# Kernel optimization log

Measured on AMD Instinct MI355X. Metric: run time of the kernel, lower is better.

The kernel has to match this reference:

```python
import jax, jax.numpy as jnp
import numpy as np

H, D_MODEL, LEN_Q, LEN_K, D_K, D_V = 16, 1024, 2048, 2048, 64, 64
BATCH = 4
SCALE = 1.0 / np.sqrt(float(D_K))


def setup_inputs() -> dict:
    key = jax.random.key(0)
    ks = jax.random.split(key, 10)
    inp = {
        "Q": jax.random.normal(ks[0], (BATCH, LEN_Q, D_MODEL), dtype=jnp.float32),
        "K": jax.random.normal(ks[1], (BATCH, LEN_K, D_MODEL), dtype=jnp.float32),
        "V": jax.random.normal(ks[2], (BATCH, LEN_K, D_MODEL), dtype=jnp.float32),
        "mask": jax.random.randint(ks[3], (BATCH, LEN_K), 0, 2, dtype=jnp.int32),
        # Linear params (torch Linear: y = x @ W.T + b); store W as [in, out].
        "Wq": jax.random.normal(ks[4], (D_MODEL, H * D_K), dtype=jnp.float32) * (1.0 / np.sqrt(D_MODEL)),
        "bq": jnp.zeros((H * D_K,), dtype=jnp.float32),
        "Wk": jax.random.normal(ks[5], (D_MODEL, H * D_K), dtype=jnp.float32) * (1.0 / np.sqrt(D_MODEL)),
        "bk": jnp.zeros((H * D_K,), dtype=jnp.float32),
        "Wv": jax.random.normal(ks[6], (D_MODEL, H * D_V), dtype=jnp.float32) * (1.0 / np.sqrt(D_MODEL)),
        "bv": jnp.zeros((H * D_V,), dtype=jnp.float32),
    }
    return inp


def reference(Q, K, V, mask, Wq, bq, Wk, bk, Wv, bv):
    B = Q.shape[0]
    # Projections -> [B, S, H, d]
    q = (Q @ Wq + bq).reshape(B, LEN_Q, H, D_K)
    k = (K @ Wk + bk).reshape(B, LEN_K, H, D_K)
    v = (V @ Wv + bv).reshape(B, LEN_K, H, D_V)
    # Scores: [B, H, len_q, len_k]
    scores = jnp.einsum("bqhd,bkhd->bhqk", q, k) * SCALE
    # Key-padding mask broadcast over heads and queries
    scores = jnp.where(mask[:, None, None, :] == 0, jnp.float32(-1e9), scores)
    alpha = jax.nn.softmax(scores, axis=-1)
    out = jnp.einsum("bhqk,bkhd->bqhd", alpha, v)  # [B, len_q, H, d_v]
    return out.reshape(B, LEN_Q, H * D_V)
```

## Files before the change

### kernel.cpp

```cpp
#include <hip/hip_runtime.h>

#define NH 16
#define DM 1024
#define SQ 2048
#define BT 4

typedef __attribute__((ext_vector_type(8))) short bf16x8;
typedef __attribute__((ext_vector_type(4))) short sh4;
typedef __attribute__((ext_vector_type(4))) float f4;
typedef __attribute__((ext_vector_type(4))) float fv4;
typedef unsigned short u16;

#define M2BIAS 23.083120654f
#define SCALE2 0.18033688f

__device__ __forceinline__ u16 f2bf(float f) {
    union { float f; unsigned u; } v; v.f = f;
    unsigned r = v.u + 0x7FFFu + ((v.u >> 16) & 1u);
    return (u16)(r >> 16);
}

__device__ __forceinline__ float fast_exp2(float x) {
#if __has_builtin(__builtin_amdgcn_exp2f)
    return __builtin_amdgcn_exp2f(x);
#else
    return exp2f(x);
#endif
}

#if __has_builtin(__builtin_amdgcn_mfma_f32_16x16x16_bf16)
#define MFMA16(a, b, c) __builtin_amdgcn_mfma_f32_16x16x16_bf16(a, b, c, 0, 0, 0)
#elif __has_builtin(__builtin_amdgcn_mfma_f32_16x16x16bf16_1k)
#define MFMA16(a, b, c) __builtin_amdgcn_mfma_f32_16x16x16bf16_1k(a, b, c, 0, 0, 0)
#else
static __device__ __forceinline__ f4 mfma16_asm(sh4 a, sh4 b, f4 c) {
    asm("v_mfma_f32_16x16x16_bf16 %0, %1, %2, %0" : "+v"(c) : "v"(a), "v"(b));
    return c;
}
#define MFMA16(a, b, c) mfma16_asm(a, b, c)
#endif

#define GLD16(gp, lp) __builtin_amdgcn_global_load_lds( \
    (const __attribute__((address_space(1))) void*)(gp), \
    (__attribute__((address_space(3))) void*)(lp), 16, 0, 0)

__global__ __launch_bounds__(256) void cvt_x(const float* __restrict__ x, u16* __restrict__ y) {
    int i = blockIdx.x * 256 + threadIdx.x;
    fv4 v = ((const fv4*)x)[i];
    sh4 r;
    r[0] = (short)f2bf(v[0]); r[1] = (short)f2bf(v[1]);
    r[2] = (short)f2bf(v[2]); r[3] = (short)f2bf(v[3]);
    ((sh4*)y)[i] = r;
}

__global__ __launch_bounds__(256) void cvt_wT(const float* __restrict__ Wsrc, u16* __restrict__ Wt) {
    __shared__ float t[64][65];
    int r0 = blockIdx.x * 64, c0 = blockIdx.y * 64;
    #pragma unroll
    for (int i = 0; i < 16; ++i) {
        int idx = i * 256 + threadIdx.x;
        int r = idx >> 6, c = idx & 63;
        t[r][c] = Wsrc[(size_t)(r0 + r) * DM + c0 + c];
    }
    __syncthreads();
    #pragma unroll
    for (int i = 0; i < 16; ++i) {
        int idx = i * 256 + threadIdx.x;
        int n = idx >> 6, k = idx & 63;
        Wt[(size_t)(c0 + n) * DM + r0 + k] = f2bf(t[k][n]);
    }
}

__global__ __launch_bounds__(256) void mk_mbias(const int* __restrict__ mask, float* __restrict__ mb) {
    int i = blockIdx.x * 256 + threadIdx.x;
    mb[i] = mask[i] ? -M2BIAS : -__builtin_inff();
}

__global__ __launch_bounds__(256) void gemm_proj(const u16* __restrict__ A, const u16* __restrict__ Bt,
                                                 const float* __restrict__ bias, u16* __restrict__ outp,
                                                 int vmode) {
    __shared__ u16 As[128 * 64];
    __shared__ u16 Bs[128 * 64];
    int tid = threadIdx.x;
    int w = tid >> 6, lane = tid & 63, quad = lane >> 4, l16 = lane & 15;
    int wm = w >> 1, wn = w & 1;
    int r8 = lane >> 3, cg = (lane & 7) ^ r8;
    const u16* Ag = A + (size_t)blockIdx.x * 128 * DM;
    const u16* Bg = Bt + (size_t)blockIdx.y * 128 * DM;

    f4 acc[4][4];
    #pragma unroll
    for (int mt = 0; mt < 4; ++mt)
        #pragma unroll
        for (int nt = 0; nt < 4; ++nt) acc[mt][nt] = f4{0.f, 0.f, 0.f, 0.f};

    for (int kt = 0; kt < 16; ++kt) {
        int kofs = kt * 64 + cg * 8;
        #pragma unroll
        for (int c = 0; c < 4; ++c) {
            int rbase = w * 32 + c * 8;
            GLD16(Ag + (size_t)(rbase + r8) * DM + kofs, &As[rbase * 64]);
            GLD16(Bg + (size_t)(rbase + r8) * DM + kofs, &Bs[rbase * 64]);
        }
        __syncthreads();
        #pragma unroll
        for (int ks = 0; ks < 2; ++ks) {
            bf16x8 afr[4], bfr[4];
            #pragma unroll
            for (int mt = 0; mt < 4; ++mt) {
                int row = wm * 64 + mt * 16 + l16;
                int ch = (ks * 4 + quad) ^ (row & 7);
                afr[mt] = *(const bf16x8*)&As[row * 64 + ch * 8];
            }
            #pragma unroll
            for (int nt = 0; nt < 4; ++nt) {
                int row = wn * 64 + nt * 16 + l16;
                int ch = (ks * 4 + quad) ^ (row & 7);
                bfr[nt] = *(const bf16x8*)&Bs[row * 64 + ch * 8];
            }
            #pragma unroll
            for (int mt = 0; mt < 4; ++mt)
                #pragma unroll
                for (int nt = 0; nt < 4; ++nt)
                    acc[mt][nt] = __builtin_amdgcn_mfma_f32_16x16x32_bf16(afr[mt], bfr[nt], acc[mt][nt], 0, 0, 0);
        }
        __syncthreads();
    }

    #pragma unroll
    for (int nt = 0; nt < 4; ++nt) {
        int ncol = blockIdx.y * 128 + wn * 64 + nt * 16 + l16;
        float bn = bias[ncol];
        int h = ncol >> 6, d = ncol & 63;
        #pragma unroll
        for (int mt = 0; mt < 4; ++mt) {
            int mbase = blockIdx.x * 128 + wm * 64 + mt * 16 + quad * 4;
            int bidx = mbase >> 11, s0 = mbase & 2047;
            if (vmode == 0) {
                size_t base = ((size_t)bidx * NH + h) * SQ;
                #pragma unroll
                for (int reg = 0; reg < 4; ++reg)
                    outp[(base + s0 + reg) * 64 + d] = f2bf(acc[mt][nt][reg] + bn);
            } else {
                sh4 pk;
                #pragma unroll
                for (int reg = 0; reg < 4; ++reg) pk[reg] = (short)f2bf(acc[mt][nt][reg] + bn);
                *(sh4*)&outp[(((size_t)bidx * NH + h) * 64 + d) * SQ + s0] = pk;
            }
        }
    }
}

__global__ __launch_bounds__(256, 4) void attn(const u16* __restrict__ qw, const u16* __restrict__ kw,
                                               const u16* __restrict__ vtw, const float* __restrict__ mbias,
                                               float* __restrict__ outp) {
    __shared__ u16 Ks[2][64 * 64];
    __shared__ u16 Vs[2][64 * 64];
    int tid = threadIdx.x;
    int w = tid >> 6, lane = tid & 63, quad = lane >> 4, l16 = lane & 15;
    int r8 = lane >> 3, sl = lane & 7;
    int bh = blockIdx.x, b = bh >> 4;
    int h = bh & 15;
    int qbase = blockIdx.y * 128 + w * 32;
    const u16* qp = qw + (size_t)bh * SQ * 64;
    const u16* kp = kw + (size_t)bh * SQ * 64;
    const u16* vp = vtw + (size_t)bh * 64 * SQ;
    const float* mbp = mbias + b * SQ;

    bf16x8 aq[2][2];
    #pragma unroll
    for (int mt = 0; mt < 2; ++mt)
        #pragma unroll
        for (int ks = 0; ks < 2; ++ks)
            aq[mt][ks] = *(const bf16x8*)&qp[(size_t)(qbase + mt * 16 + l16) * 64 + ks * 32 + quad * 8];

    f4 o[2][4];
    float lrow[2] = {0.f, 0.f};
    #pragma unroll
    for (int mt = 0; mt < 2; ++mt)
        #pragma unroll
        for (int nt = 0; nt < 4; ++nt) o[mt][nt] = f4{0.f, 0.f, 0.f, 0.f};

    auto stage = [&](int buf, int k0) {
        #pragma unroll
        for (int j = 0; j < 2; ++j) {
            int row = w * 16 + j * 8 + r8;
            int gsl = sl ^ (row & 7);
            GLD16(kp + (size_t)(k0 + row) * 64 + gsl * 8, &Ks[buf][(w * 16 + j * 8) * 64]);
            GLD16(vp + (size_t)row * SQ + k0 + gsl * 8, &Vs[buf][(w * 16 + j * 8) * 64]);
        }
    };

    stage(0, 0);
    for (int kb = 0; kb < 32; ++kb) {
        int buf = kb & 1;
        int k0 = kb * 64;
        __syncthreads();
        fv4 bias4[4];
        #pragma unroll
        for (int kt = 0; kt < 4; ++kt)
            bias4[kt] = *(const fv4*)&mbp[k0 + kt * 16 + quad * 4];
        if (kb + 1 < 32) stage(buf ^ 1, k0 + 64);

        bf16x8 bk[4][2];
        #pragma unroll
        for (int kt = 0; kt < 4; ++kt)
            #pragma unroll
            for (int ks = 0; ks < 2; ++ks) {
                int r = kt * 16 + l16;
                int slot = (ks * 4 + quad) ^ (r & 7);
                bk[kt][ks] = *(const bf16x8*)&Ks[buf][r * 64 + slot * 8];
            }
        f4 S[4][2];
        #pragma unroll
        for (int kt = 0; kt < 4; ++kt)
            #pragma unroll
            for (int mt = 0; mt < 2; ++mt) {
                f4 s = f4{0.f, 0.f, 0.f, 0.f};
                s = __builtin_amdgcn_mfma_f32_16x16x32_bf16(bk[kt][0], aq[mt][0], s, 0, 0, 0);
                s = __builtin_amdgcn_mfma_f32_16x16x32_bf16(bk[kt][1], aq[mt][1], s, 0, 0, 0);
                S[kt][mt] = s;
            }
        #pragma unroll
        for (int kt = 0; kt < 4; ++kt) {
            sh4 pa[2];
            #pragma unroll
            for (int mt = 0; mt < 2; ++mt) {
                f4 s = S[kt][mt];
                float p0 = fast_exp2(s[0] * SCALE2 + bias4[kt][0]);
                float p1 = fast_exp2(s[1] * SCALE2 + bias4[kt][1]);
                float p2 = fast_exp2(s[2] * SCALE2 + bias4[kt][2]);
                float p3 = fast_exp2(s[3] * SCALE2 + bias4[kt][3]);
                lrow[mt] += (p0 + p1) + (p2 + p3);
                pa[mt][0] = (short)(__float_as_uint(p0) >> 16);
                pa[mt][1] = (short)(__float_as_uint(p1) >> 16);
                pa[mt][2] = (short)(__float_as_uint(p2) >> 16);
                pa[mt][3] = (short)(__float_as_uint(p3) >> 16);
            }
            sh4 bv[4];
            #pragma unroll
            for (int nt = 0; nt < 4; ++nt) {
                int row = nt * 16 + l16;
                int ch = (2 * kt + (quad >> 1)) ^ (row & 7);
                bv[nt] = *(const sh4*)&Vs[buf][row * 64 + ch * 8 + (quad & 1) * 4];
            }
            #pragma unroll
            for (int mt = 0; mt < 2; ++mt)
                #pragma unroll
                for (int nt = 0; nt < 4; ++nt)
                    o[mt][nt] = MFMA16(pa[mt], bv[nt], o[mt][nt]);
        }
    }

    #pragma unroll
    for (int mt = 0; mt < 2; ++mt) {
        float v = lrow[mt];
        v += __shfl_xor(v, 16);
        v += __shfl_xor(v, 32);
        #pragma unroll
        for (int reg = 0; reg < 4; ++reg) {
            float inv = 1.f / __shfl(v, quad * 4 + reg);
            int row = qbase + mt * 16 + quad * 4 + reg;
            size_t obase = ((size_t)b * SQ + row) * DM + h * 64;
            #pragma unroll
            for (int nt = 0; nt < 4; ++nt)
                outp[obase + nt * 16 + l16] = o[mt][nt][reg] * inv;
        }
    }
}

extern "C" void kernel_launch(void* const* d_in, const int* in_sizes, int n_in,
                              void* d_out, int out_size, void* d_ws, size_t ws_size,
                              hipStream_t stream) {
    (void)in_sizes; (void)n_in; (void)out_size; (void)ws_size;
    const float* Q  = (const float*)d_in[0];
    const float* K  = (const float*)d_in[1];
    const float* V  = (const float*)d_in[2];
    const int* mask = (const int*)d_in[3];
    const float* Wq = (const float*)d_in[4];
    const float* bq = (const float*)d_in[5];
    const float* Wk = (const float*)d_in[6];
    const float* bk = (const float*)d_in[7];
    const float* Wv = (const float*)d_in[8];
    const float* bv = (const float*)d_in[9];
    float* out = (float*)d_out;
    char* ws = (char*)d_ws;
    u16* q_ws = (u16*)(ws);
    u16* k_ws = (u16*)(ws + (size_t)16 * 1024 * 1024);
    u16* v_ws = (u16*)(ws + (size_t)32 * 1024 * 1024);
    u16* xbuf = (u16*)(ws + (size_t)48 * 1024 * 1024);
    u16* wbuf = (u16*)(ws + (size_t)64 * 1024 * 1024);
    float* mb = (float*)(ws + (size_t)48 * 1024 * 1024);

    dim3 gGemm(64, 8), gW(16, 16);
    cvt_x<<<8192, 256, 0, stream>>>(Q, xbuf);
    cvt_wT<<<gW, 256, 0, stream>>>(Wq, wbuf);
    gemm_proj<<<gGemm, 256, 0, stream>>>(xbuf, wbuf, bq, q_ws, 0);
    cvt_x<<<8192, 256, 0, stream>>>(K, xbuf);
    cvt_wT<<<gW, 256, 0, stream>>>(Wk, wbuf);
    gemm_proj<<<gGemm, 256, 0, stream>>>(xbuf, wbuf, bk, k_ws, 0);
    cvt_x<<<8192, 256, 0, stream>>>(V, xbuf);
    cvt_wT<<<gW, 256, 0, stream>>>(Wv, wbuf);
    gemm_proj<<<gGemm, 256, 0, stream>>>(xbuf, wbuf, bv, v_ws, 1);
    mk_mbias<<<32, 256, 0, stream>>>(mask, mb);
    attn<<<dim3(64, 16), 256, 0, stream>>>(q_ws, k_ws, v_ws, mb, out);
}
```

Measured before the change: 337.9 us.

## Fuse fp32-to-bf16 activation conversion into a single batched QKV projection GEMM

Drops the separate cvt_x passes. The projection GEMM now loads fp32 activations straight into LDS and rounds them to bf16 in registers. The three weight transposes and the three projection GEMMs are each batched into one launch through blockIdx.z, and Q/K now use swapped MFMA operands so they can store vectorised outputs. The attention kernel precomputes LDS offsets and staging pointers, unrolls the K-loop by two, and packs P with a byte-permute. This removes the activation conversion round-trip through memory and several launches, at the cost of doubling LDS traffic for A tiles and higher LDS use per GEMM block.

```diff
diff --git a/kernel.cpp b/kernel.cpp
--- a/kernel.cpp
+++ b/kernel.cpp
@@ -10,6 +10,7 @@
 typedef __attribute__((ext_vector_type(4))) float f4;
 typedef __attribute__((ext_vector_type(4))) float fv4;
 typedef unsigned short u16;
+typedef unsigned int u32;
 
 #define M2BIAS 23.083120654f
 #define SCALE2 0.18033688f
@@ -44,17 +45,20 @@
     (const __attribute__((address_space(1))) void*)(gp), \
     (__attribute__((address_space(3))) void*)(lp), 16, 0, 0)
 
-__global__ __launch_bounds__(256) void cvt_x(const float* __restrict__ x, u16* __restrict__ y) {
-    int i = blockIdx.x * 256 + threadIdx.x;
-    fv4 v = ((const fv4*)x)[i];
-    sh4 r;
-    r[0] = (short)f2bf(v[0]); r[1] = (short)f2bf(v[1]);
-    r[2] = (short)f2bf(v[2]); r[3] = (short)f2bf(v[3]);
-    ((sh4*)y)[i] = r;
-}
-
-__global__ __launch_bounds__(256) void cvt_wT(const float* __restrict__ Wsrc, u16* __restrict__ Wt) {
+__device__ __forceinline__ u32 pk_trunc(float lo, float hi) {
+    return __builtin_amdgcn_perm(__float_as_uint(hi), __float_as_uint(lo), 0x07060302u);
+}
+__device__ __forceinline__ u32 pk_round(float lo, float hi) {
+    u32 a = __float_as_uint(lo) + 0x8000u;
+    u32 b = __float_as_uint(hi) + 0x8000u;
+    return __builtin_amdgcn_perm(b, a, 0x07060302u);
+}
+
+__global__ __launch_bounds__(256) void cvt_wT(const float* __restrict__ W0, const float* __restrict__ W1,
+                                              const float* __restrict__ W2, u16* __restrict__ Wt) {
     __shared__ float t[64][65];
+    const float* Wsrc = blockIdx.z == 0 ? W0 : (blockIdx.z == 1 ? W1 : W2);
+    u16* dst = Wt + (size_t)blockIdx.z * DM * DM;
     int r0 = blockIdx.x * 64, c0 = blockIdx.y * 64;
     #pragma unroll
     for (int i = 0; i < 16; ++i) {
@@ -67,7 +71,7 @@
     for (int i = 0; i < 16; ++i) {
         int idx = i * 256 + threadIdx.x;
         int n = idx >> 6, k = idx & 63;
-        Wt[(size_t)(c0 + n) * DM + r0 + k] = f2bf(t[k][n]);
+        dst[(size_t)(c0 + n) * DM + r0 + k] = f2bf(t[k][n]);
     }
 }
 
@@ -76,31 +80,47 @@
     mb[i] = mask[i] ? -M2BIAS : -__builtin_inff();
 }
 
-__global__ __launch_bounds__(256) void gemm_proj(const u16* __restrict__ A, const u16* __restrict__ Bt,
-                                                 const float* __restrict__ bias, u16* __restrict__ outp,
-                                                 int vmode) {
-    __shared__ u16 As[128 * 64];
+__global__ __launch_bounds__(256) void gemm_fused(const float* __restrict__ Xq, const float* __restrict__ Xk,
+                                                  const float* __restrict__ Xv, const u16* __restrict__ Wt,
+                                                  const float* __restrict__ bqv, const float* __restrict__ bkv,
+                                                  const float* __restrict__ bvv,
+                                                  u16* __restrict__ qo, u16* __restrict__ ko, u16* __restrict__ vo) {
+    __shared__ float Asf[128 * 64];
     __shared__ u16 Bs[128 * 64];
+    int z = blockIdx.z;
+    const float* A    = z == 0 ? Xq : (z == 1 ? Xk : Xv);
+    const float* bias = z == 0 ? bqv : (z == 1 ? bkv : bvv);
+    u16* outp         = z == 0 ? qo : (z == 1 ? ko : vo);
+    const u16* Bg = Wt + (size_t)z * DM * DM + (size_t)blockIdx.y * 128 * DM;
+    const float* Ag = A + (size_t)blockIdx.x * 128 * DM;
+    bool vt = (z == 2);
+
     int tid = threadIdx.x;
     int w = tid >> 6, lane = tid & 63, quad = lane >> 4, l16 = lane & 15;
     int wm = w >> 1, wn = w & 1;
     int r8 = lane >> 3, cg = (lane & 7) ^ r8;
-    const u16* Ag = A + (size_t)blockIdx.x * 128 * DM;
-    const u16* Bg = Bt + (size_t)blockIdx.y * 128 * DM;
+    int l4 = lane >> 4, s16 = lane & 15;
 
     f4 acc[4][4];
     #pragma unroll
-    for (int mt = 0; mt < 4; ++mt)
-        #pragma unroll
-        for (int nt = 0; nt < 4; ++nt) acc[mt][nt] = f4{0.f, 0.f, 0.f, 0.f};
+    for (int i = 0; i < 4; ++i)
+        #pragma unroll
+        for (int j = 0; j < 4; ++j) acc[i][j] = f4{0.f, 0.f, 0.f, 0.f};
+
+    int aswz = ((l16 & 7) << 1) | (l16 >> 3);
 
     for (int kt = 0; kt < 16; ++kt) {
-        int kofs = kt * 64 + cg * 8;
+        #pragma unroll
+        for (int c = 0; c < 8; ++c) {
+            int rl = w * 32 + c * 4 + l4;
+            int rm = rl & 15;
+            int g = s16 ^ (((rm & 7) << 1) | (rm >> 3));
+            GLD16(Ag + (size_t)rl * DM + kt * 64 + g * 4, &Asf[(w * 32 + c * 4) * 64]);
+        }
         #pragma unroll
         for (int c = 0; c < 4; ++c) {
             int rbase = w * 32 + c * 8;
-            GLD16(Ag + (size_t)(rbase + r8) * DM + kofs, &As[rbase * 64]);
-            GLD16(Bg + (size_t)(rbase + r8) * DM + kofs, &Bs[rbase * 64]);
+            GLD16(Bg + (size_t)(rbase + r8) * DM + kt * 64 + cg * 8, &Bs[rbase * 64]);
         }
         __syncthreads();
         #pragma unroll
@@ -109,8 +129,15 @@
             #pragma unroll
             for (int mt = 0; mt < 4; ++mt) {
                 int row = wm * 64 + mt * 16 + l16;
-                int ch = (ks * 4 + quad) ^ (row & 7);
-                afr[mt] = *(const bf16x8*)&As[row * 64 + ch * 8];
+                int s0 = (ks * 8 + quad * 2) ^ aswz;
+                f4 a0 = *(const f4*)&Asf[row * 64 + s0 * 4];
+                f4 a1 = *(const f4*)&Asf[row * 64 + (s0 ^ 1) * 4];
+                union { bf16x8 v; u32 u[4]; } af;
+                af.u[0] = pk_round(a0[0], a0[1]);
+                af.u[1] = pk_round(a0[2], a0[3]);
+                af.u[2] = pk_round(a1[0], a1[1]);
+                af.u[3] = pk_round(a1[2], a1[3]);
+                afr[mt] = af.v;
             }
             #pragma unroll
             for (int nt = 0; nt < 4; ++nt) {
@@ -119,29 +146,41 @@
                 bfr[nt] = *(const bf16x8*)&Bs[row * 64 + ch * 8];
             }
             #pragma unroll
-            for (int mt = 0; mt < 4; ++mt)
+            for (int i = 0; i < 4; ++i)
                 #pragma unroll
-                for (int nt = 0; nt < 4; ++nt)
-                    acc[mt][nt] = __builtin_amdgcn_mfma_f32_16x16x32_bf16(afr[mt], bfr[nt], acc[mt][nt], 0, 0, 0);
+                for (int j = 0; j < 4; ++j)
+                    acc[i][j] = __builtin_amdgcn_mfma_f32_16x16x32_bf16(
+                        vt ? afr[i] : bfr[i], vt ? bfr[j] : afr[j], acc[i][j], 0, 0, 0);
         }
         __syncthreads();
     }
 
-    #pragma unroll
-    for (int nt = 0; nt < 4; ++nt) {
-        int ncol = blockIdx.y * 128 + wn * 64 + nt * 16 + l16;
-        float bn = bias[ncol];
-        int h = ncol >> 6, d = ncol & 63;
-        #pragma unroll
-        for (int mt = 0; mt < 4; ++mt) {
-            int mbase = blockIdx.x * 128 + wm * 64 + mt * 16 + quad * 4;
-            int bidx = mbase >> 11, s0 = mbase & 2047;
-            if (vmode == 0) {
-                size_t base = ((size_t)bidx * NH + h) * SQ;
+    if (!vt) {
+        #pragma unroll
+        for (int nt = 0; nt < 4; ++nt) {
+            int ncb = blockIdx.y * 128 + wn * 64 + nt * 16 + quad * 4;
+            fv4 bn4 = *(const fv4*)&bias[ncb];
+            int h = ncb >> 6, d0 = ncb & 63;
+            #pragma unroll
+            for (int mt = 0; mt < 4; ++mt) {
+                int s = blockIdx.x * 128 + wm * 64 + mt * 16 + l16;
+                int bidx = s >> 11, srow = s & 2047;
+                sh4 pk;
                 #pragma unroll
-                for (int reg = 0; reg < 4; ++reg)
-                    outp[(base + s0 + reg) * 64 + d] = f2bf(acc[mt][nt][reg] + bn);
-            } else {
+                for (int reg = 0; reg < 4; ++reg) pk[reg] = (short)f2bf(acc[nt][mt][reg] + bn4[reg]);
+                *(sh4*)&outp[(((size_t)bidx * NH + h) * SQ + srow) * 64 + d0] = pk;
+            }
+        }
+    } else {
+        #pragma unroll
+        for (int nt = 0; nt < 4; ++nt) {
+            int ncol = blockIdx.y * 128 + wn * 64 + nt * 16 + l16;
+            float bn = bias[ncol];
+            int h = ncol >> 6, d = ncol & 63;
+            #pragma unroll
+            for (int mt = 0; mt < 4; ++mt) {
+                int mbase = blockIdx.x * 128 + wm * 64 + mt * 16 + quad * 4;
+                int bidx = mbase >> 11, s0 = mbase & 2047;
                 sh4 pk;
                 #pragma unroll
                 for (int reg = 0; reg < 4; ++reg) pk[reg] = (short)f2bf(acc[mt][nt][reg] + bn);
@@ -165,7 +204,7 @@
     const u16* qp = qw + (size_t)bh * SQ * 64;
     const u16* kp = kw + (size_t)bh * SQ * 64;
     const u16* vp = vtw + (size_t)bh * 64 * SQ;
-    const float* mbp = mbias + b * SQ;
+    const float* mbq = mbias + b * SQ + quad * 4;
 
     bf16x8 aq[2][2];
     #pragma unroll
@@ -174,6 +213,31 @@
         for (int ks = 0; ks < 2; ++ks)
             aq[mt][ks] = *(const bf16x8*)&qp[(size_t)(qbase + mt * 16 + l16) * 64 + ks * 32 + quad * 8];
 
+    int bk_off[4][2], bv_off[4][4];
+    #pragma unroll
+    for (int kt = 0; kt < 4; ++kt) {
+        int r = kt * 16 + l16;
+        #pragma unroll
+        for (int ks = 0; ks < 2; ++ks)
+            bk_off[kt][ks] = r * 64 + (((ks * 4 + quad) ^ (l16 & 7)) * 8);
+        #pragma unroll
+        for (int nt = 0; nt < 4; ++nt) {
+            int row = nt * 16 + l16;
+            int ch = (2 * kt + (quad >> 1)) ^ (l16 & 7);
+            bv_off[kt][nt] = row * 64 + ch * 8 + (quad & 1) * 4;
+        }
+    }
+    int gsl = sl ^ r8;
+    int krow0 = w * 16 + r8, krow1 = krow0 + 8;
+    const u16* kp0 = kp + (size_t)krow0 * 64 + gsl * 8;
+    const u16* kp1 = kp + (size_t)krow1 * 64 + gsl * 8;
+    const u16* vp0 = vp + (size_t)krow0 * SQ + gsl * 8;
+    const u16* vp1 = vp + (size_t)krow1 * SQ + gsl * 8;
+    u16* KsW0 = &Ks[0][(w * 16) * 64];       u16* KsW0b = &Ks[0][(w * 16 + 8) * 64];
+    u16* VsW0 = &Vs[0][(w * 16) * 64];       u16* VsW0b = &Vs[0][(w * 16 + 8) * 64];
+    u16* KsW1 = &Ks[1][(w * 16) * 64];       u16* KsW1b = &Ks[1][(w * 16 + 8) * 64];
+    u16* VsW1 = &Vs[1][(w * 16) * 64];       u16* VsW1b = &Vs[1][(w * 16 + 8) * 64];
+
     f4 o[2][4];
     float lrow[2] = {0.f, 0.f};
     #pragma unroll
@@ -181,17 +245,10 @@
         #pragma unroll
         for (int nt = 0; nt < 4; ++nt) o[mt][nt] = f4{0.f, 0.f, 0.f, 0.f};
 
-    auto stage = [&](int buf, int k0) {
-        #pragma unroll
-        for (int j = 0; j < 2; ++j) {
-            int row = w * 16 + j * 8 + r8;
-            int gsl = sl ^ (row & 7);
-            GLD16(kp + (size_t)(k0 + row) * 64 + gsl * 8, &Ks[buf][(w * 16 + j * 8) * 64]);
-            GLD16(vp + (size_t)row * SQ + k0 + gsl * 8, &Vs[buf][(w * 16 + j * 8) * 64]);
-        }
-    };
-
-    stage(0, 0);
+    GLD16(kp0, KsW0); GLD16(kp1, KsW0b);
+    GLD16(vp0, VsW0); GLD16(vp1, VsW0b);
+
+    #pragma unroll 2
     for (int kb = 0; kb < 32; ++kb) {
         int buf = kb & 1;
         int k0 = kb * 64;
@@ -199,18 +256,26 @@
         fv4 bias4[4];
         #pragma unroll
         for (int kt = 0; kt < 4; ++kt)
-            bias4[kt] = *(const fv4*)&mbp[k0 + kt * 16 + quad * 4];
-        if (kb + 1 < 32) stage(buf ^ 1, k0 + 64);
-
+            bias4[kt] = *(const fv4*)&mbq[k0 + kt * 16];
+        if (kb + 1 < 32) {
+            int kn = k0 + 64;
+            if (buf == 0) {
+                GLD16(kp0 + kn * 64, KsW1); GLD16(kp1 + kn * 64, KsW1b);
+                GLD16(vp0 + kn, VsW1);      GLD16(vp1 + kn, VsW1b);
+            } else {
+                GLD16(kp0 + kn * 64, KsW0); GLD16(kp1 + kn * 64, KsW0b);
+                GLD16(vp0 + kn, VsW0);      GLD16(vp1 + kn, VsW0b);
+            }
+        }
+
+        const u16* Kb = Ks[buf];
+        const u16* Vb = Vs[buf];
         bf16x8 bk[4][2];
         #pragma unroll
         for (int kt = 0; kt < 4; ++kt)
             #pragma unroll
-            for (int ks = 0; ks < 2; ++ks) {
-                int r = kt * 16 + l16;
-                int slot = (ks * 4 + quad) ^ (r & 7);
-                bk[kt][ks] = *(const bf16x8*)&Ks[buf][r * 64 + slot * 8];
-            }
+            for (int ks = 0; ks < 2; ++ks)
+                bk[kt][ks] = *(const bf16x8*)&Kb[bk_off[kt][ks]];
         f4 S[4][2];
         #pragma unroll
         for (int kt = 0; kt < 4; ++kt)
@@ -232,18 +297,15 @@
                 float p2 = fast_exp2(s[2] * SCALE2 + bias4[kt][2]);
                 float p3 = fast_exp2(s[3] * SCALE2 + bias4[kt][3]);
                 lrow[mt] += (p0 + p1) + (p2 + p3);
-                pa[mt][0] = (short)(__float_as_uint(p0) >> 16);
-                pa[mt][1] = (short)(__float_as_uint(p1) >> 16);
-                pa[mt][2] = (short)(__float_as_uint(p2) >> 16);
-                pa[mt][3] = (short)(__float_as_uint(p3) >> 16);
+                union { sh4 v; u32 u[2]; } pk;
+                pk.u[0] = pk_trunc(p0, p1);
+                pk.u[1] = pk_trunc(p2, p3);
+                pa[mt] = pk.v;
             }
             sh4 bv[4];
             #pragma unroll
-            for (int nt = 0; nt < 4; ++nt) {
-                int row = nt * 16 + l16;
-                int ch = (2 * kt + (quad >> 1)) ^ (row & 7);
-                bv[nt] = *(const sh4*)&Vs[buf][row * 64 + ch * 8 + (quad & 1) * 4];
-            }
+            for (int nt = 0; nt < 4; ++nt)
+                bv[nt] = *(const sh4*)&Vb[bv_off[kt][nt]];
             #pragma unroll
             for (int mt = 0; mt < 2; ++mt)
                 #pragma unroll
@@ -288,20 +350,11 @@
     u16* q_ws = (u16*)(ws);
     u16* k_ws = (u16*)(ws + (size_t)16 * 1024 * 1024);
     u16* v_ws = (u16*)(ws + (size_t)32 * 1024 * 1024);
-    u16* xbuf = (u16*)(ws + (size_t)48 * 1024 * 1024);
-    u16* wbuf = (u16*)(ws + (size_t)64 * 1024 * 1024);
-    float* mb = (float*)(ws + (size_t)48 * 1024 * 1024);
-
-    dim3 gGemm(64, 8), gW(16, 16);
-    cvt_x<<<8192, 256, 0, stream>>>(Q, xbuf);
-    cvt_wT<<<gW, 256, 0, stream>>>(Wq, wbuf);
-    gemm_proj<<<gGemm, 256, 0, stream>>>(xbuf, wbuf, bq, q_ws, 0);
-    cvt_x<<<8192, 256, 0, stream>>>(K, xbuf);
-    cvt_wT<<<gW, 256, 0, stream>>>(Wk, wbuf);
-    gemm_proj<<<gGemm, 256, 0, stream>>>(xbuf, wbuf, bk, k_ws, 0);
-    cvt_x<<<8192, 256, 0, stream>>>(V, xbuf);
-    cvt_wT<<<gW, 256, 0, stream>>>(Wv, wbuf);
-    gemm_proj<<<gGemm, 256, 0, stream>>>(xbuf, wbuf, bv, v_ws, 1);
+    u16* wbuf = (u16*)(ws + (size_t)48 * 1024 * 1024);
+    float* mb = (float*)(ws + (size_t)54 * 1024 * 1024);
+
+    cvt_wT<<<dim3(16, 16, 3), 256, 0, stream>>>(Wq, Wk, Wv, wbuf);
     mk_mbias<<<32, 256, 0, stream>>>(mask, mb);
+    gemm_fused<<<dim3(64, 8, 3), 256, 0, stream>>>(Q, K, V, wbuf, bq, bk, bv, q_ws, k_ws, v_ws);
     attn<<<dim3(64, 16), 256, 0, stream>>>(q_ws, k_ws, v_ws, mb, out);
 }
```

Result: slower. 349.3 us (+3.4%).
